# Kernel tuning notes

Measured on AMD Instinct MI355X. Metric: run time of the kernel, lower is better.

## Reference

```python
import jax, jax.numpy as jnp
import numpy as np
from jax import lax

K = 3            # RFAConv kernel size
CIN = 66         # RFAConv in_channel = c2/2 + 2
UP = 64          # up channel count = c2/2
BN_EPS = 1e-5


def conv2d(x, w, stride=1, padding=0, groups=1, bias=None):
    out = lax.conv_general_dilated(
        x, w, (stride, stride), [(padding, padding), (padding, padding)],
        dimension_numbers=("NCHW", "OIHW", "NCHW"), feature_group_count=groups)
    if bias is not None:
        out = out + bias[None, :, None, None]
    return out


def avgpool3(x):
    # AvgPool2d(kernel=3, pad=1, stride=1), count_include_pad=True -> /9 everywhere
    s = lax.reduce_window(x, 0.0, lax.add, (1, 1, 3, 3), (1, 1, 1, 1),
                          [(0, 0), (0, 0), (1, 1), (1, 1)])
    return s / 9.0


def setup_inputs() -> dict:
    key = jax.random.key(0)
    ks = jax.random.split(key, 8)
    c1, c2 = 64, 128
    inp = {
        "x": jax.random.normal(ks[0], (8, c1, 256, 256), jnp.float32),
        "w_squeeze": jax.random.normal(ks[1], (c2, 4 * c1, 1, 1), jnp.float32) * 0.05,
        "w_gw": jax.random.normal(ks[2], (CIN * K * K, 1, 1, 1), jnp.float32) * 0.3,
        "w_gf": jax.random.normal(ks[3], (CIN * K * K, 1, K, K), jnp.float32) * 0.3,
        "bn_gamma": jnp.ones((CIN * K * K,), jnp.float32),
        "bn_beta": jnp.zeros((CIN * K * K,), jnp.float32),
        "bn_mean": jnp.zeros((CIN * K * K,), jnp.float32),
        "bn_var": jnp.ones((CIN * K * K,), jnp.float32),
        "w_conv": jax.random.normal(ks[4], (UP, CIN, K, K), jnp.float32) * 0.05,
        "b_conv": jnp.zeros((UP,), jnp.float32),
    }
    return inp


def reference(x, w_squeeze, w_gw, w_gf, bn_gamma, bn_beta, bn_mean, bn_var,
              w_conv, b_conv):
    # space_to_depth: [B,C,H,W] -> [B,4C,H/2,W/2]
    x = jnp.concatenate([x[..., ::2, ::2], x[..., 1::2, ::2],
                         x[..., ::2, 1::2], x[..., 1::2, 1::2]], axis=1)
    # squeeze0: 1x1 conv 4*c1 -> c2
    x = conv2d(x, w_squeeze)
    up, low = x[:, :UP], x[:, UP:]

    # AddCoords (with_r=False): append normalized xx (width) and yy (height)
    b, _, h, w = up.shape
    xx = (jnp.arange(w, dtype=up.dtype) / (w - 1) * 2.0 - 1.0)
    yy = (jnp.arange(h, dtype=up.dtype) / (h - 1) * 2.0 - 1.0)
    xx = jnp.broadcast_to(xx[None, None, None, :], (b, 1, h, w))
    yy = jnp.broadcast_to(yy[None, None, :, None], (b, 1, h, w))
    up = jnp.concatenate([up, xx, yy], axis=1)   # [b, 66, h, w]

    # RFAConv
    weight = conv2d(avgpool3(up), w_gw, groups=CIN)          # [b, 594, h, w]
    weight = jax.nn.softmax(weight.reshape(b, CIN, K * K, h, w), axis=2)

    feat = conv2d(up, w_gf, stride=1, padding=1, groups=CIN)  # [b, 594, h, w]
    scale = bn_gamma / jnp.sqrt(bn_var + BN_EPS)
    shift = bn_beta - bn_mean * scale
    feat = jax.nn.relu(feat * scale[None, :, None, None] + shift[None, :, None, None])
    feat = feat.reshape(b, CIN, K * K, h, w)

    wd = feat * weight
    # rearrange 'b c (n1 n2) h w -> b c (h n1) (w n2)'
    wd = wd.reshape(b, CIN, K, K, h, w).transpose(0, 1, 4, 2, 5, 3)
    wd = wd.reshape(b, CIN, h * K, w * K)
    up = conv2d(wd, w_conv, stride=K, bias=b_conv)            # [b, 64, h, w]

    y = jnp.concatenate([up, low], axis=1)                    # [b, 128, h, w]
    # channel shuffle: gather even channels then odd channels
    bb, n, hh, ww = y.shape
    y = y.reshape(bb, n // 2, 2, hh, ww)
    return jnp.concatenate([y[:, :, 0], y[:, :, 1]], axis=1)
```

## Files before the change

### kernel.cpp

```cpp
#include <hip/hip_runtime.h>
#include <math.h>

typedef __attribute__((ext_vector_type(8))) short short8;
typedef __attribute__((ext_vector_type(4))) float f32x4;

#define CIN 66
#define BN_EPS 1e-5f

#define PLROW 136
#define PLN   17680

#define CO_F     ((size_t)4587520)
#define BSQ_U16  ((size_t)16777216)
#define BSQ_CNT  32768
#define BF_U16   (BSQ_U16 + BSQ_CNT)
#define BF_CNT   40960
#define SC_F     ((size_t)8425472)
#define SH_F     (SC_F + 594)
#define GW2_F    (SH_F + 594)
#define GF2_F    (GW2_F + 594)

static __device__ __forceinline__ unsigned short f2bf(float f) {
    unsigned u = __float_as_uint(f);
    u += 0x7fffu + ((u >> 16) & 1u);
    return (unsigned short)(u >> 16);
}
static __device__ __forceinline__ unsigned pack2(float lo, float hi) {
    return __builtin_amdgcn_perm(__float_as_uint(hi) + 0x8000u,
                                 __float_as_uint(lo) + 0x8000u, 0x07060302u);
}

__global__ void prep_kernel(const float* __restrict__ w_squeeze,
                            const float* __restrict__ gamma,
                            const float* __restrict__ beta,
                            const float* __restrict__ mean,
                            const float* __restrict__ var,
                            const float* __restrict__ w_gw,
                            const float* __restrict__ w_gf,
                            const float* __restrict__ w_conv,
                            float* __restrict__ ws)
{
    unsigned short* wsu = (unsigned short*)ws;
    const int tid = blockIdx.x * blockDim.x + threadIdx.x;
    const int nth = gridDim.x * blockDim.x;

    for (int idx = tid; idx < BSQ_CNT; idx += nth) {
        int j = idx & 7, lane = (idx >> 3) & 63, r = idx >> 9;
        int nt = r & 7, kc = r >> 3;
        int k = kc * 32 + ((lane >> 4) << 3) + j;
        int n = nt * 16 + (lane & 15);
        wsu[BSQ_U16 + idx] = f2bf(w_squeeze[n * 256 + k]);
    }
    for (int idx = tid; idx < BF_CNT; idx += nth) {
        int j = idx & 7, lane = (idx >> 3) & 63, r = idx >> 9;
        int nt = r & 3, ks = r >> 2;
        int kp = ks * 32 + ((lane >> 4) << 3) + j;
        int chunk = kp / 160, rem = kp - chunk * 160;
        int wvv = rem / 40, s = rem - wvv * 40;
        int n = nt * 16 + (lane & 15);
        float v = 0.f;
        if (s < 36) v = w_conv[n * 594 + chunk * 144 + wvv * 36 + s];
        wsu[BF_U16 + idx] = f2bf(v);
    }
    for (int i = tid; i < CIN * 9; i += nth) {
        float sc = gamma[i] / sqrtf(var[i] + BN_EPS);
        ws[SC_F + i] = sc;
        ws[SH_F + i] = beta[i] - mean[i] * sc;
    }
    for (int i = tid; i < CIN * 9; i += nth)
        ws[GW2_F + i] = w_gw[i] * 0.16029944573f;
    for (int i = tid; i < CIN * 81; i += nth) {
        int cj = i / 9;
        float sc = gamma[cj] * rsqrtf(var[cj] + BN_EPS);
        ws[GF2_F + i] = w_gf[i] * sc;
    }
    for (int idx = tid; idx < 512 * 648; idx += nth) {
        int plane = idx / 648, r = idx - plane * 648;
        unsigned* pb = (unsigned*)(wsu + (size_t)plane * PLN);
        if (r < 68)       pb[r] = 0u;
        else if (r < 136) pb[8772 + (r - 68)] = 0u;
        else {
            int rr = (r - 136) >> 2, k = (r - 136) & 3;
            pb[(rr + 1) * 68 + (k < 2 ? k : 64 + k)] = 0u;
        }
    }
    if (tid < 65536) {
        const int pix = tid & 16383;
        const int g   = tid >> 14;
        const int h = pix >> 7, w = pix & 127;
        float fsA[9], fsB[9];
#pragma unroll
        for (int c = 0; c < 2; ++c) {
            const int cu = 64 + c;
            float n[9];
#pragma unroll
            for (int dy = 0; dy < 3; ++dy)
#pragma unroll
                for (int dx = 0; dx < 3; ++dx) {
                    const int gy = h - 1 + dy, gx = w - 1 + dx;
                    const bool ok = ((unsigned)gy < 128u) & ((unsigned)gx < 128u);
                    const float v = (c == 0) ? (gx * (2.f / 127.f) - 1.f)
                                             : (gy * (2.f / 127.f) - 1.f);
                    n[dy * 3 + dx] = ok ? v : 0.f;
                }
            const float p = (n[0]+n[1]+n[2]+n[3]+n[4]+n[5]+n[6]+n[7]+n[8]) * (1.f/9.f);
            const float* gw = w_gw + cu * 9;
            const float* gf = w_gf + cu * 81;
            float e[9], se = 0.f;
#pragma unroll
            for (int j = 0; j < 9; ++j) { e[j] = __expf(p * gw[j]); se += e[j]; }
            const float sinv = 1.f / se;
            float* fs = c ? fsB : fsA;
#pragma unroll
            for (int j = 0; j < 9; ++j) {
                float cv = 0.f;
#pragma unroll
                for (int i = 0; i < 9; ++i) cv = fmaf(n[i], gf[j * 9 + i], cv);
                const float sc = gamma[cu * 9 + j] / sqrtf(var[cu * 9 + j] + BN_EPS);
                const float sh = beta[cu * 9 + j] - mean[cu * 9 + j] * sc;
                const float f = fmaf(cv, sc, sh);
                fs[j] = fmaxf(f, 0.f) * (e[j] * sinv);
            }
        }
#pragma unroll 1
        for (int oc = g * 16; oc < g * 16 + 16; ++oc) {
            const float* wc = w_conv + oc * 594;
            float s = 0.f;
#pragma unroll
            for (int j = 0; j < 9; ++j)
                s = fmaf(fsA[j], wc[576 + j], fmaf(fsB[j], wc[585 + j], s));
            ws[CO_F + (size_t)oc * 16384 + pix] = s;
        }
    }
}

__global__ __launch_bounds__(256, 7) void squeeze_mfma(
    const float* __restrict__ x,
    float* __restrict__ wsp,
    float* __restrict__ out)
{
    __shared__ __align__(16) uint2 As2[32 * 32 * 2];

    const int bx  = blockIdx.x;
    const int b   = bx & 7;
    const int pos = bx >> 3;
    const int h   = pos >> 2;
    const int w0  = (pos & 3) * 32;
    const int tid  = threadIdx.x;
    const int lane = tid & 63;
    const int wv   = tid >> 6;
    const int oct  = tid >> 5;
    const int hf   = (tid >> 4) & 1;
    const int pp   = tid & 15;

    float4 v[2][4];
#pragma unroll
    for (int gy = 0; gy < 2; ++gy)
#pragma unroll
        for (int i = 0; i < 4; ++i)
            v[gy][i] = *(const float4*)(x +
                (size_t)(b * 64 + oct * 8 + hf * 4 + i) * 65536 +
                (2 * h + gy) * 256 + 2 * w0 + 4 * pp);

#pragma unroll
    for (int gy = 0; gy < 2; ++gy)
#pragma unroll
        for (int gx = 0; gx < 2; ++gx)
#pragma unroll
            for (int p = 0; p < 2; ++p) {
                const int comp = p * 2 + gx;
                uint2 u;
                u.x = pack2(((const float*)&v[gy][0])[comp], ((const float*)&v[gy][1])[comp]);
                u.y = pack2(((const float*)&v[gy][2])[comp], ((const float*)&v[gy][3])[comp]);
                As2[(((gy + 2 * gx) * 8 + oct) * 32 + 2 * pp + p) * 2 + hf] = u;
            }

    const unsigned short* bsq = (const unsigned short*)wsp + BSQ_U16;
    short8 b0 = *(const short8*)(bsq + (size_t)((2 * wv + 0) * 64 + lane) * 8);
    short8 b1 = *(const short8*)(bsq + (size_t)((2 * wv + 1) * 64 + lane) * 8);

    __syncthreads();

    const uint4* As4 = (const uint4*)As2;
    const int q = lane >> 4, m = lane & 15;
    f32x4 acc[2][2];
#pragma unroll
    for (int mt = 0; mt < 2; ++mt)
#pragma unroll
        for (int j = 0; j < 2; ++j) acc[mt][j] = (f32x4){0.f, 0.f, 0.f, 0.f};

#pragma unroll
    for (int ks = 0; ks < 8; ++ks) {
        short8 nb0, nb1;
        if (ks < 7) {
            nb0 = *(const short8*)(bsq + (size_t)(((ks + 1) * 8 + 2 * wv + 0) * 64 + lane) * 8);
            nb1 = *(const short8*)(bsq + (size_t)(((ks + 1) * 8 + 2 * wv + 1) * 64 + lane) * 8);
        }
#pragma unroll
        for (int mt = 0; mt < 2; ++mt) {
            short8 a = *(const short8*)&As4[(ks * 4 + q) * 32 + mt * 16 + m];
            acc[mt][0] = __builtin_amdgcn_mfma_f32_16x16x32_bf16(a, b0, acc[mt][0], 0, 0, 0);
            acc[mt][1] = __builtin_amdgcn_mfma_f32_16x16x32_bf16(a, b1, acc[mt][1], 0, 0, 0);
        }
        if (ks < 7) { b0 = nb0; b1 = nb1; }
    }

    if (wv < 2) {
        unsigned short* upw = (unsigned short*)wsp;
#pragma unroll
        for (int j = 0; j < 2; ++j) {
            const int oc = (2 * wv + j) * 16 + m;
#pragma unroll
            for (int mt = 0; mt < 2; ++mt) {
                uint2 st;
                st.x = pack2(acc[mt][j][0], acc[mt][j][1]);
                st.y = pack2(acc[mt][j][2], acc[mt][j][3]);
                *(uint2*)(upw + (size_t)(b * 64 + oc) * PLN + (size_t)(h + 1) * PLROW
                          + (w0 + mt * 16 + q * 4 + 4)) = st;
            }
        }
    } else {
#pragma unroll
        for (int j = 0; j < 2; ++j) {
            const int oc = (2 * wv + j) * 16 + m;
            const int lc = oc - 64;
            const int ch = (lc & 1) ? (96 + ((lc - 1) >> 1)) : (32 + (lc >> 1));
#pragma unroll
            for (int mt = 0; mt < 2; ++mt) {
                float4 st = {acc[mt][j][0], acc[mt][j][1], acc[mt][j][2], acc[mt][j][3]};
                *(float4*)(out + ((size_t)(b * 128 + ch) * 128 + h) * 128
                           + (w0 + mt * 16 + q * 4)) = st;
            }
        }
    }
}

__device__ __forceinline__ void fs_from_n2(
    int cu, const float n[9],
    const float* __restrict__ gw2, const float* __restrict__ gf2,
    const float* __restrict__ shp, float fs[9])
{
    const float s = ((n[0] + n[1]) + (n[2] + n[3])) + ((n[4] + n[5]) + (n[6] + n[7])) + n[8];
    const float* gw = gw2 + cu * 9;
    const float* gf = gf2 + cu * 81;
    const float* sh = shp + cu * 9;
    float e[9], se = 0.f;
#pragma unroll
    for (int j = 0; j < 9; ++j) { e[j] = __builtin_amdgcn_exp2f(s * gw[j]); se += e[j]; }
    const float sinv = __builtin_amdgcn_rcpf(se);
#pragma unroll
    for (int j = 0; j < 9; ++j) {
        float cv = sh[j];
#pragma unroll
        for (int i = 0; i < 9; ++i) cv = fmaf(n[i], gf[j * 9 + i], cv);
        fs[j] = fmaxf(cv, 0.f) * (e[j] * sinv);
    }
}

__device__ __forceinline__ void pack_into(unsigned* pk, int ci, const float fs[9], float& carry)
{
    const int off = 9 * ci;
    if ((ci & 1) == 0) {
#pragma unroll
        for (int t = 0; t < 4; ++t) pk[off / 2 + t] = pack2(fs[2 * t], fs[2 * t + 1]);
        carry = fs[8];
    } else {
        pk[(off - 1) / 2] = pack2(carry, fs[0]);
#pragma unroll
        for (int t = 0; t < 4; ++t) pk[(off + 1) / 2 + t] = pack2(fs[1 + 2 * t], fs[2 + 2 * t]);
    }
}

__device__ __forceinline__ void chunk_loads4(
    int cbase, int lane, int h0, int w0,
    const unsigned short* __restrict__ upb, uint2 vr[4][3])
{
    const int px = lane & 7, py = lane >> 3;
    const size_t rowoff = (size_t)(h0 + py) * PLROW + (size_t)((w0 + px + 3) & ~1);
#pragma unroll
    for (int ci = 0; ci < 4; ++ci) {
        const int cu = __builtin_amdgcn_readfirstlane(cbase + ci);
        const unsigned short* cb = upb + (size_t)cu * PLN + rowoff;
#pragma unroll
        for (int dy = 0; dy < 3; ++dy)
            vr[ci][dy] = *(const uint2*)(cb + dy * PLROW);
    }
}

__device__ __forceinline__ void chunk_compute4(
    int cbase, int lane, const uint2 vr[4][3],
    const float* __restrict__ gw2, const float* __restrict__ gf2,
    const float* __restrict__ shp, unsigned pk[20])
{
    const unsigned shf = (lane & 1) ? 0u : 16u;
    float carry = 0.f;
#pragma unroll
    for (int ci = 0; ci < 4; ++ci) {
        const int cu = __builtin_amdgcn_readfirstlane(cbase + ci);
        float n[9];
#pragma unroll
        for (int dy = 0; dy < 3; ++dy) {
            const uint2 vv = vr[ci][dy];
            unsigned long long t = (((unsigned long long)vv.y) << 32) | vv.x;
            t >>= shf;
            n[dy * 3 + 0] = __uint_as_float((unsigned)t << 16);
            n[dy * 3 + 1] = __uint_as_float((unsigned)t & 0xffff0000u);
            n[dy * 3 + 2] = __uint_as_float((unsigned)(t >> 32) << 16);
        }
        float fs[9];
        fs_from_n2(cu, n, gw2, gf2, shp, fs);
        pack_into(pk, ci, fs, carry);
    }
    pk[18] = 0u; pk[19] = 0u;
}

__device__ __forceinline__ void do_mfma5(
    int bbase, const uint4* As, const unsigned short* __restrict__ bfw,
    int wv, int lane, f32x4 acc[2][2])
{
    const int q = lane >> 4, m = lane & 15;
    const int ntb = (wv >> 1) * 2;
    const int pt0 = (wv & 1) * 2;
#pragma unroll
    for (int ks = 0; ks < 5; ++ks) {
        short8 b0 = *(const short8*)(bfw + (size_t)(((bbase + ks) * 4 + ntb + 0) * 64 + lane) * 8);
        short8 b1 = *(const short8*)(bfw + (size_t)(((bbase + ks) * 4 + ntb + 1) * 64 + lane) * 8);
#pragma unroll
        for (int mt = 0; mt < 2; ++mt) {
            short8 a = *(const short8*)&As[(ks * 4 + q) * 64 + (pt0 + mt) * 16 + m];
            acc[mt][0] = __builtin_amdgcn_mfma_f32_16x16x32_bf16(a, b0, acc[mt][0], 0, 0, 0);
            acc[mt][1] = __builtin_amdgcn_mfma_f32_16x16x32_bf16(a, b1, acc[mt][1], 0, 0, 0);
        }
    }
}

__global__ __launch_bounds__(256, 8) void fused_mfma(
    const float* __restrict__ wsp,
    const float* __restrict__ b_conv,
    float* __restrict__ out)
{
    __shared__ uint4 As[20 * 64];

    const int bx = blockIdx.x;
    const int b  = bx & 7;
    const int t  = bx >> 3;
    const int w0 = (t & 15) * 8;
    const int h0 = ((t >> 4) & 15) * 8;
    const int tid = threadIdx.x, lane = tid & 63, wv = tid >> 6;

    const unsigned short* upb = (const unsigned short*)wsp + (size_t)b * 64 * PLN;
    const float* gw2 = wsp + GW2_F;
    const float* gf2 = wsp + GF2_F;
    const float* shp = wsp + SH_F;
    const unsigned short* bfw = (const unsigned short*)wsp + BF_U16;

    f32x4 acc[2][2];
#pragma unroll
    for (int mt = 0; mt < 2; ++mt)
#pragma unroll
        for (int j = 0; j < 2; ++j) acc[mt][j] = (f32x4){0.f, 0.f, 0.f, 0.f};

    uint2 vr[4][3];
    unsigned pk[20];

    chunk_loads4(wv * 4, lane, h0, w0, upb, vr);
    chunk_compute4(wv * 4, lane, vr, gw2, gf2, shp, pk);
#pragma unroll
    for (int kb = 0; kb < 5; ++kb)
        As[(5 * wv + kb) * 64 + lane] =
            (uint4){pk[4 * kb], pk[4 * kb + 1], pk[4 * kb + 2], pk[4 * kb + 3]};
    __syncthreads();

#pragma unroll
    for (int c = 0; c < 4; ++c) {
        if (c < 3) chunk_loads4((c + 1) * 16 + wv * 4, lane, h0, w0, upb, vr);
        do_mfma5(c * 5, As, bfw, wv, lane, acc);
        if (c < 3) {
            chunk_compute4((c + 1) * 16 + wv * 4, lane, vr, gw2, gf2, shp, pk);
            __syncthreads();
#pragma unroll
            for (int kb = 0; kb < 5; ++kb)
                As[(5 * wv + kb) * 64 + lane] =
                    (uint4){pk[4 * kb], pk[4 * kb + 1], pk[4 * kb + 2], pk[4 * kb + 3]};
            __syncthreads();
        }
    }

    const int q = lane >> 4, m = lane & 15;
    const int ntb = (wv >> 1) * 2, pt0 = (wv & 1) * 2;
    const float* co = wsp + CO_F;
#pragma unroll
    for (int mt = 0; mt < 2; ++mt)
#pragma unroll
        for (int j = 0; j < 2; ++j) {
            const int oc = (ntb + j) * 16 + m;
            const int ch = (oc & 1) ? (64 + (oc >> 1)) : (oc >> 1);
            const int row = h0 + (pt0 + mt) * 2 + (q >> 1);
            const int col = w0 + (q & 1) * 4;
            const size_t pix = (size_t)row * 128 + col;
            const float4 cv = *(const float4*)(co + (size_t)oc * 16384 + pix);
            const float bias = b_conv[oc];
            float4 st = { acc[mt][j][0] + bias + cv.x,
                          acc[mt][j][1] + bias + cv.y,
                          acc[mt][j][2] + bias + cv.z,
                          acc[mt][j][3] + bias + cv.w };
            *(float4*)(out + (size_t)(b * 128 + ch) * 16384 + pix) = st;
        }
}

extern "C" void kernel_launch(void* const* d_in, const int* in_sizes, int n_in,
                              void* d_out, int out_size, void* d_ws, size_t ws_size,
                              hipStream_t stream)
{
    const float* x         = (const float*)d_in[0];
    const float* w_squeeze = (const float*)d_in[1];
    const float* w_gw      = (const float*)d_in[2];
    const float* w_gf      = (const float*)d_in[3];
    const float* gamma     = (const float*)d_in[4];
    const float* beta      = (const float*)d_in[5];
    const float* mean      = (const float*)d_in[6];
    const float* var       = (const float*)d_in[7];
    const float* w_conv    = (const float*)d_in[8];
    const float* b_conv    = (const float*)d_in[9];
    float* out = (float*)d_out;
    float* ws  = (float*)d_ws;

    prep_kernel<<<256, 256, 0, stream>>>(w_squeeze, gamma, beta, mean, var,
                                         w_gw, w_gf, w_conv, ws);
    squeeze_mfma<<<4096, 256, 0, stream>>>(x, ws, out);
    fused_mfma<<<2048, 256, 0, stream>>>(ws, b_conv, out);
}
```

Baseline: 331.0 us.

## Double fused kernel tile to 16x8 pixels with 512-thread blocks

The fused RFA kernel now processes a 16x8 pixel tile per block with 8 waves instead of an 8x8 tile with 4 waves. Each wave produces features for 4 channels of one 8x8 half, and the MFMA stage splits waves into 4 M-tiles by 2 N-tile pairs. Each block then reuses every B-fragment load from the conv weights across twice as many pixels, halving the weight traffic per pixel. In exchange LDS doubles to 40KB per block, occupancy hints drop to 6 blocks of 512 threads, and there are half as many blocks.

```diff
diff --git a/kernel.cpp b/kernel.cpp
--- a/kernel.cpp
+++ b/kernel.cpp
@@ -56,10 +56,10 @@
         int nt = r & 3, ks = r >> 2;
         int kp = ks * 32 + ((lane >> 4) << 3) + j;
         int chunk = kp / 160, rem = kp - chunk * 160;
-        int wvv = rem / 40, s = rem - wvv * 40;
+        int cq = rem / 40, s = rem - cq * 40;
         int n = nt * 16 + (lane & 15);
         float v = 0.f;
-        if (s < 36) v = w_conv[n * 594 + chunk * 144 + wvv * 36 + s];
+        if (s < 36) v = w_conv[n * 594 + chunk * 144 + cq * 36 + s];
         wsu[BF_U16 + idx] = f2bf(v);
     }
     for (int i = tid; i < CIN * 9; i += nth) {
@@ -272,11 +272,11 @@
 }
 
 __device__ __forceinline__ void chunk_loads4(
-    int cbase, int lane, int h0, int w0,
+    int cbase, int lane, int hb, int w0,
     const unsigned short* __restrict__ upb, uint2 vr[4][3])
 {
     const int px = lane & 7, py = lane >> 3;
-    const size_t rowoff = (size_t)(h0 + py) * PLROW + (size_t)((w0 + px + 3) & ~1);
+    const size_t rowoff = (size_t)(hb + py) * PLROW + (size_t)((w0 + px + 3) & ~1);
 #pragma unroll
     for (int ci = 0; ci < 4; ++ci) {
         const int cu = __builtin_amdgcn_readfirstlane(cbase + ci);
@@ -314,39 +314,43 @@
     pk[18] = 0u; pk[19] = 0u;
 }
 
-__device__ __forceinline__ void do_mfma5(
+__device__ __forceinline__ void do_mfma5w(
     int bbase, const uint4* As, const unsigned short* __restrict__ bfw,
     int wv, int lane, f32x4 acc[2][2])
 {
     const int q = lane >> 4, m = lane & 15;
-    const int ntb = (wv >> 1) * 2;
-    const int pt0 = (wv & 1) * 2;
+    const int ntb = (wv >> 2) * 2;
+    const int mtb = (wv & 3) * 2;
 #pragma unroll
     for (int ks = 0; ks < 5; ++ks) {
         short8 b0 = *(const short8*)(bfw + (size_t)(((bbase + ks) * 4 + ntb + 0) * 64 + lane) * 8);
         short8 b1 = *(const short8*)(bfw + (size_t)(((bbase + ks) * 4 + ntb + 1) * 64 + lane) * 8);
 #pragma unroll
         for (int mt = 0; mt < 2; ++mt) {
-            short8 a = *(const short8*)&As[(ks * 4 + q) * 64 + (pt0 + mt) * 16 + m];
+            short8 a = *(const short8*)&As[(ks * 4 + q) * 128 + (mtb + mt) * 16 + m];
             acc[mt][0] = __builtin_amdgcn_mfma_f32_16x16x32_bf16(a, b0, acc[mt][0], 0, 0, 0);
             acc[mt][1] = __builtin_amdgcn_mfma_f32_16x16x32_bf16(a, b1, acc[mt][1], 0, 0, 0);
         }
     }
 }
 
-__global__ __launch_bounds__(256, 8) void fused_mfma(
+__global__ __launch_bounds__(512, 6) void fused_mfma(
     const float* __restrict__ wsp,
     const float* __restrict__ b_conv,
     float* __restrict__ out)
 {
-    __shared__ uint4 As[20 * 64];
+    __shared__ uint4 As[20 * 128];
 
     const int bx = blockIdx.x;
     const int b  = bx & 7;
     const int t  = bx >> 3;
     const int w0 = (t & 15) * 8;
-    const int h0 = ((t >> 4) & 15) * 8;
+    const int h0 = (t >> 4) * 16;
     const int tid = threadIdx.x, lane = tid & 63, wv = tid >> 6;
+    const int ph = wv >> 2;
+    const int cq = wv & 3;
+    const int hb = h0 + ph * 8;
+    const int p  = ph * 64 + lane;
 
     const unsigned short* upb = (const unsigned short*)wsp + (size_t)b * 64 * PLN;
     const float* gw2 = wsp + GW2_F;
@@ -363,31 +367,31 @@
     uint2 vr[4][3];
     unsigned pk[20];
 
-    chunk_loads4(wv * 4, lane, h0, w0, upb, vr);
-    chunk_compute4(wv * 4, lane, vr, gw2, gf2, shp, pk);
+    chunk_loads4(cq * 4, lane, hb, w0, upb, vr);
+    chunk_compute4(cq * 4, lane, vr, gw2, gf2, shp, pk);
 #pragma unroll
     for (int kb = 0; kb < 5; ++kb)
-        As[(5 * wv + kb) * 64 + lane] =
+        As[(cq * 5 + kb) * 128 + p] =
             (uint4){pk[4 * kb], pk[4 * kb + 1], pk[4 * kb + 2], pk[4 * kb + 3]};
     __syncthreads();
 
 #pragma unroll
     for (int c = 0; c < 4; ++c) {
-        if (c < 3) chunk_loads4((c + 1) * 16 + wv * 4, lane, h0, w0, upb, vr);
-        do_mfma5(c * 5, As, bfw, wv, lane, acc);
+        if (c < 3) chunk_loads4((c + 1) * 16 + cq * 4, lane, hb, w0, upb, vr);
+        do_mfma5w(c * 5, As, bfw, wv, lane, acc);
         if (c < 3) {
-            chunk_compute4((c + 1) * 16 + wv * 4, lane, vr, gw2, gf2, shp, pk);
+            chunk_compute4((c + 1) * 16 + cq * 4, lane, vr, gw2, gf2, shp, pk);
             __syncthreads();
 #pragma unroll
             for (int kb = 0; kb < 5; ++kb)
-                As[(5 * wv + kb) * 64 + lane] =
+                As[(cq * 5 + kb) * 128 + p] =
                     (uint4){pk[4 * kb], pk[4 * kb + 1], pk[4 * kb + 2], pk[4 * kb + 3]};
             __syncthreads();
         }
     }
 
     const int q = lane >> 4, m = lane & 15;
-    const int ntb = (wv >> 1) * 2, pt0 = (wv & 1) * 2;
+    const int ntb = (wv >> 2) * 2, mtb = (wv & 3) * 2;
     const float* co = wsp + CO_F;
 #pragma unroll
     for (int mt = 0; mt < 2; ++mt)
@@ -395,8 +399,9 @@
         for (int j = 0; j < 2; ++j) {
             const int oc = (ntb + j) * 16 + m;
             const int ch = (oc & 1) ? (64 + (oc >> 1)) : (oc >> 1);
-            const int row = h0 + (pt0 + mt) * 2 + (q >> 1);
-            const int col = w0 + (q & 1) * 4;
+            const int p0 = (mtb + mt) * 16 + q * 4;
+            const int row = h0 + (p0 >> 3);
+            const int col = w0 + (p0 & 7);
             const size_t pix = (size_t)row * 128 + col;
             const float4 cv = *(const float4*)(co + (size_t)oc * 16384 + pix);
             const float bias = b_conv[oc];
@@ -428,5 +433,5 @@
     prep_kernel<<<256, 256, 0, stream>>>(w_squeeze, gamma, beta, mean, var,
                                          w_gw, w_gf, w_conv, ws);
     squeeze_mfma<<<4096, 256, 0, stream>>>(x, ws, out);
-    fused_mfma<<<2048, 256, 0, stream>>>(ws, b_conv, out);
-}
+    fused_mfma<<<1024, 512, 0, stream>>>(ws, b_conv, out);
+}
```

After: 333.4 us. No clear change (+0.7%).
